# Kernel optimization log

Measured on AMD Instinct MI355X. Metric: run time of the kernel, lower is better.

Reference implementation:

```python
import jax, jax.numpy as jnp
import numpy as np

EPS = 1e-5

def conv2d(x, w, stride=1, padding=0, bias=None):
    out = jax.lax.conv_general_dilated(
        x, w, (stride, stride), [(padding, padding), (padding, padding)],
        dimension_numbers=('NCHW', 'OIHW', 'NCHW'))
    if bias is not None:
        out = out + bias[None, :, None, None]
    return out

def bn_relu(x, gamma, beta, mean, var):
    scale = gamma / jnp.sqrt(var + EPS)
    return jax.nn.relu(x * scale[None, :, None, None]
                       + (beta - mean * scale)[None, :, None, None])

def deform_conv(x, wp, bp, wc, ks, pad, stride):
    # Canonical DeformConv2d (v1, modulation=False) from pytorch-deform-conv-v2.
    b, c, H, W = x.shape
    N = ks * ks
    offset = conv2d(x, wp, stride=stride, padding=1, bias=bp)        # (b,2N,h,w)
    h, w = offset.shape[2], offset.shape[3]
    xp = jnp.pad(x, ((0, 0), (0, 0), (pad, pad), (pad, pad)))        # zero_padding
    Hp, Wp = H + 2 * pad, W + 2 * pad
    off = offset.transpose(0, 2, 3, 1)                               # (b,h,w,2N)
    rng = jnp.arange(-(ks - 1) // 2, (ks - 1) // 2 + 1, dtype=x.dtype)
    pnx, pny = jnp.meshgrid(rng, rng, indexing='ij')
    pnx, pny = pnx.reshape(-1), pny.reshape(-1)                      # (N,)
    p0x = jnp.arange(1, h * stride + 1, stride, dtype=x.dtype)       # torch starts at 1
    p0y = jnp.arange(1, w * stride + 1, stride, dtype=x.dtype)
    px = p0x[None, :, None, None] + pnx[None, None, None, :] + off[..., :N]  # (b,h,w,N)
    py = p0y[None, None, :, None] + pny[None, None, None, :] + off[..., N:]
    qx0 = jnp.floor(jax.lax.stop_gradient(px))
    qy0 = jnp.floor(jax.lax.stop_gradient(py))
    qx0c = jnp.clip(qx0, 0, Hp - 1).astype(jnp.int32)
    qx1c = jnp.clip(qx0 + 1, 0, Hp - 1).astype(jnp.int32)
    qy0c = jnp.clip(qy0, 0, Wp - 1).astype(jnp.int32)
    qy1c = jnp.clip(qy0 + 1, 0, Wp - 1).astype(jnp.int32)
    pxc = jnp.clip(px, 0, Hp - 1)
    pyc = jnp.clip(py, 0, Wp - 1)
    fx0 = qx0c.astype(x.dtype); fx1 = qx1c.astype(x.dtype)
    fy0 = qy0c.astype(x.dtype); fy1 = qy1c.astype(x.dtype)
    g_lt = (1 + (fx0 - pxc)) * (1 + (fy0 - pyc))
    g_rb = (1 - (fx1 - pxc)) * (1 - (fy1 - pyc))
    g_lb = (1 + (fx0 - pxc)) * (1 - (fy1 - pyc))
    g_rt = (1 - (fx1 - pxc)) * (1 + (fy0 - pyc))
    xf = xp.reshape(b, c, Hp * Wp)
    def gather(qx, qy):
        idx = (qx * Wp + qy).reshape(b, 1, h * w * N)
        return jnp.take_along_axis(xf, idx, axis=2).reshape(b, c, h, w, N)
    x_off = (g_lt[:, None] * gather(qx0c, qy0c)
             + g_rb[:, None] * gather(qx1c, qy1c)
             + g_lb[:, None] * gather(qx0c, qy1c)
             + g_rt[:, None] * gather(qx1c, qy0c))                   # (b,c,h,w,N)
    # stride=ks conv over the reshaped (h*ks, w*ks) map == einsum over sample slot n
    return jnp.einsum('bchwn,ocn->bohw', x_off, wc.reshape(wc.shape[0], c, N))

def setup_inputs() -> dict:
    key = jax.random.key(0)
    ks = iter(jax.random.split(key, 40))
    def nrm(shape, scale):
        return jax.random.normal(next(ks), shape, dtype=jnp.float32) * scale
    def he(shape):  # fan_in = prod of all but first dim
        return nrm(shape, float(np.sqrt(2.0 / np.prod(shape[1:]))))
    def bn(c):
        return (jnp.ones((c,), jnp.float32) + nrm((c,), 0.05),  # gamma
                nrm((c,), 0.05),                                 # beta
                nrm((c,), 0.1),                                  # running mean
                jax.random.uniform(next(ks), (c,), jnp.float32, 0.5, 1.5))  # var
    inp = {'x': jax.random.normal(next(ks), (256, 3, 32, 32), dtype=jnp.float32)}
    inp['w1'] = he((32, 3, 3, 3)); inp['b1'] = nrm((32,), 0.01)
    inp['g1'], inp['be1'], inp['m1'], inp['v1'] = bn(32)
    inp['wp2'] = nrm((18, 32, 3, 3), 0.01); inp['bp2'] = nrm((18,), 0.001)
    inp['wc2'] = he((64, 32, 3, 3))
    inp['g2'], inp['be2'], inp['m2'], inp['v2'] = bn(64)
    inp['wp3'] = nrm((18, 64, 3, 3), 0.01); inp['bp3'] = nrm((18,), 0.001)
    inp['wc3'] = he((128, 64, 3, 3))
    inp['g3'], inp['be3'], inp['m3'], inp['v3'] = bn(128)
    inp['wp4'] = nrm((18, 128, 3, 3), 0.01); inp['bp4'] = nrm((18,), 0.001)
    inp['wc4'] = he((128, 128, 3, 3))
    inp['g4'], inp['be4'], inp['m4'], inp['v4'] = bn(128)
    inp['wcls'] = nrm((100, 128), float(1.0 / np.sqrt(128)))
    inp['bcls'] = nrm((100,), 0.01)
    return inp

def reference(x, w1, b1, g1, be1, m1, v1,
              wp2, bp2, wc2, g2, be2, m2, v2,
              wp3, bp3, wc3, g3, be3, m3, v3,
              wp4, bp4, wc4, g4, be4, m4, v4,
              wcls, bcls):
    h = bn_relu(conv2d(x, w1, stride=1, padding=1, bias=b1), g1, be1, m1, v1)   # (b,32,32,32)
    h = bn_relu(deform_conv(h, wp2, bp2, wc2, 3, 1, 2), g2, be2, m2, v2)        # (b,64,16,16)
    h = bn_relu(deform_conv(h, wp3, bp3, wc3, 3, 1, 1), g3, be3, m3, v3)        # (b,128,16,16)
    h = bn_relu(deform_conv(h, wp4, bp4, wc4, 3, 1, 2), g4, be4, m4, v4)        # (b,128,8,8)
    h = jnp.mean(h, axis=(2, 3))                                                # avg_pool2d(8) -> (b,128)
    return h @ wcls.T + bcls[None, :]
```

## Files before the change

### kernel.cpp

```cpp
#include <hip/hip_runtime.h>
#include <math.h>

#define BN_EPS 1e-5f

typedef __attribute__((ext_vector_type(4))) float f4;
typedef __attribute__((ext_vector_type(4))) int i4v;
typedef __attribute__((ext_vector_type(8))) short short8;
typedef __attribute__((ext_vector_type(4))) float f32x4;

__device__ inline unsigned short f2bf(float f) {
    unsigned int u = __builtin_bit_cast(unsigned int, f);
    return (unsigned short)((u + 0x7FFFu + ((u >> 16) & 1u)) >> 16);
}
__device__ inline float blo(int u) { return __builtin_bit_cast(float, (int)(u << 16)); }
__device__ inline float bhi(int u) { return __builtin_bit_cast(float, (int)(u & 0xffff0000)); }
__device__ inline int pkbf_fast(float hi, float lo) {
    unsigned uh = __builtin_bit_cast(unsigned, hi) + 0x8000u;
    unsigned ul = __builtin_bit_cast(unsigned, lo) + 0x8000u;
    return (int)__builtin_amdgcn_perm(uh, ul, 0x07060302u);
}

struct CvtSeg { const float* src; unsigned short* dst; int oreal, c, kpad, end; };
struct CvtArgs { CvtSeg s[7]; };

__global__ __launch_bounds__(256)
void cvt_all(CvtArgs a)
{
    int idx = blockIdx.x * 256 + threadIdx.x;
    int base = 0;
    #pragma unroll
    for (int i = 0; i < 7; ++i) {
        if (idx < a.s[i].end) {
            int local = idx - base;
            int kpad = a.s[i].kpad, c = a.s[i].c;
            int o = local / kpad, k = local - o * kpad;
            unsigned short val = 0;
            if (o < a.s[i].oreal && k < 9 * c) {
                int n = k / c, cc = k - n * c;
                val = f2bf(a.s[i].src[(o * c + cc) * 9 + n]);
            }
            a.s[i].dst[local] = val;
            return;
        }
        base = a.s[i].end;
    }
}

__global__ __launch_bounds__(256)
void conv1_tile(const float* __restrict__ x, const unsigned short* __restrict__ wq,
                const float* __restrict__ bias, const float* __restrict__ g,
                const float* __restrict__ be, const float* __restrict__ m,
                const float* __restrict__ v, unsigned short* __restrict__ out)
{
    __shared__ __align__(16) float img[3072];
    __shared__ __align__(16) unsigned short wt[32 * 40];
    __shared__ float scb[32], shb[32];
    const int tid = threadIdx.x;
    const int b = blockIdx.x >> 2;
    const int qtr = blockIdx.x & 3;
    if (tid < 32) {
        float sc = g[tid] * rsqrtf(v[tid] + BN_EPS);
        scb[tid] = sc;
        shb[tid] = be[tid] - m[tid] * sc + bias[tid] * sc;
    }
    *(ushort4*)&wt[(tid >> 3) * 40 + (tid & 7) * 4] =
        *(const ushort4*)(wq + (tid >> 3) * 32 + (tid & 7) * 4);
    const float* xb = x + (size_t)b * 3072;
    #pragma unroll
    for (int r = 0; r < 3; ++r) {
        int idx = r * 256 + tid;
        *(f4*)&img[idx * 4] = *(const f4*)(xb + idx * 4);
    }
    __syncthreads();
    const int wid = tid >> 6, lane = tid & 63, quad = lane >> 4, m16 = lane & 15;
    short8 af0 = *(const short8*)&wt[m16 * 40 + quad * 8];
    short8 af1 = *(const short8*)&wt[(16 + m16) * 40 + quad * 8];
    #pragma unroll
    for (int it = 0; it < 4; ++it) {
        int pix = qtr * 256 + it * 64 + wid * 16 + m16;
        int i = pix >> 5, j = pix & 31;
        short8 bfrag;
        #pragma unroll
        for (int jj = 0; jj < 8; ++jj) {
            int k = quad * 8 + jj;
            float val = 0.f;
            if (k < 27) {
                int n = k / 3, c = k - n * 3;
                int u = i - 1 + n / 3, vv = j - 1 + n % 3;
                if (u >= 0 && u < 32 && vv >= 0 && vv < 32)
                    val = img[c * 1024 + u * 32 + vv];
            }
            bfrag[jj] = (short)f2bf(val);
        }
        f32x4 a0 = {0.f,0.f,0.f,0.f}, a1 = {0.f,0.f,0.f,0.f};
        a0 = __builtin_amdgcn_mfma_f32_16x16x32_bf16(af0, bfrag, a0, 0, 0, 0);
        a1 = __builtin_amdgcn_mfma_f32_16x16x32_bf16(af1, bfrag, a1, 0, 0, 0);
        unsigned short* op = out + ((size_t)b * 1024 + pix) * 32;
        ushort4 s0, s1;
        #pragma unroll
        for (int rr = 0; rr < 4; ++rr) {
            int o0 = quad * 4 + rr, o1 = 16 + quad * 4 + rr;
            ((unsigned short*)&s0)[rr] = f2bf(fmaxf(fmaf(a0[rr], scb[o0], shb[o0]), 0.f));
            ((unsigned short*)&s1)[rr] = f2bf(fmaxf(fmaf(a1[rr], scb[o1], shb[o1]), 0.f));
        }
        *(ushort4*)(op + quad * 4) = s0;
        *(ushort4*)(op + 16 + quad * 4) = s1;
    }
}

template<int C, int OREAL, int OPAD, int H, int W, int OH, int OW, int S,
         int MTILE, bool DEF, bool BN>
__global__ __launch_bounds__(256, 4)
void dconv(const unsigned short* __restrict__ xact, const float* __restrict__ offp,
           const unsigned short* __restrict__ wq,
           const float* __restrict__ q0, const float* __restrict__ q1,
           const float* __restrict__ q2, const float* __restrict__ q3,
           void* __restrict__ outv)
{
    constexpr int K = C * 9;
    constexpr int KCH = C / 32;
    constexpr int OSPLIT = (OPAD >= 64) ? 4 : 2;
    constexpr int G = 4 / OSPLIT;
    constexpr int OT = OPAD / (16 * OSPLIT);
    constexpr int PW = MTILE / G;
    constexpr int ST = PW / 16;
    constexpr int CP = C + 8;
    constexpr int GL = C / 8;
    constexpr int NGRP = 256 / GL;
    constexpr int OHW = OH * OW;
    constexpr int HWC = H * W * C;
    constexpr int Hp = H + 2, Wp = W + 2;
    static_assert(PW % 16 == 0 && OT >= 1, "tiling");

    __shared__ __align__(16) unsigned short xo[2][MTILE * CP];
    __shared__ __align__(16) i4v tab_i[DEF ? MTILE : 1][9];
    __shared__ __align__(16) f4  tab_w[DEF ? MTILE : 1][9];
    __shared__ int tab_o[DEF ? 1 : MTILE][9];
    __shared__ int tab_m[DEF ? 1 : MTILE][9];
    __shared__ int imgb[MTILE];
    __shared__ float scb[OPAD], shb[OPAD];

    const int tid = threadIdx.x;
    const int p0 = blockIdx.x * MTILE;

    if (tid < MTILE) imgb[tid] = ((p0 + tid) / OHW) * HWC;
    if (BN) {
        for (int o = tid; o < OREAL; o += 256) {
            float sc = q0[o] * rsqrtf(q3[o] + BN_EPS);
            scb[o] = sc;
            shb[o] = q1[o] - q2[o] * sc;
        }
    } else {
        for (int o = tid; o < OREAL; o += 256) scb[o] = q0[o];
    }

    for (int e = tid; e < MTILE * 9; e += 256) {
        int lp = e / 9, n = e % 9;
        int p = p0 + lp;
        int rem = p % OHW;
        int i = rem / OW, j = rem % OW;
        if constexpr (DEF) {
            float ox = offp[(size_t)p * 18 + n];
            float oy = offp[(size_t)p * 18 + 9 + n];
            float px = (float)(i * S + n / 3) + ox;
            float py = (float)(j * S + n % 3) + oy;
            int qx0 = (int)floorf(px), qy0 = (int)floorf(py);
            int x0 = min(max(qx0, 0), Hp - 1), x1 = min(max(qx0 + 1, 0), Hp - 1);
            int y0 = min(max(qy0, 0), Wp - 1), y1 = min(max(qy0 + 1, 0), Wp - 1);
            float pxc = fminf(fmaxf(px, 0.f), (float)(Hp - 1));
            float pyc = fminf(fmaxf(py, 0.f), (float)(Wp - 1));
            float gx0 = 1.f + ((float)x0 - pxc), gx1 = 1.f - ((float)x1 - pxc);
            float gy0 = 1.f + ((float)y0 - pyc), gy1 = 1.f - ((float)y1 - pyc);
            int u0 = x0 - 1, u1 = x1 - 1, v0 = y0 - 1, v1 = y1 - 1;
            bool k0 = (u0 >= 0 && u0 < H && v0 >= 0 && v0 < W);
            bool k1 = (u1 >= 0 && u1 < H && v1 >= 0 && v1 < W);
            bool k2 = (u0 >= 0 && u0 < H && v1 >= 0 && v1 < W);
            bool k3 = (u1 >= 0 && u1 < H && v0 >= 0 && v0 < W);
            i4v ti; f4 tw;
            ti[0] = k0 ? (u0 * W + v0) * C : 0;  tw[0] = k0 ? gx0 * gy0 : 0.f;
            ti[1] = k1 ? (u1 * W + v1) * C : 0;  tw[1] = k1 ? gx1 * gy1 : 0.f;
            ti[2] = k2 ? (u0 * W + v1) * C : 0;  tw[2] = k2 ? gx0 * gy1 : 0.f;
            ti[3] = k3 ? (u1 * W + v0) * C : 0;  tw[3] = k3 ? gx1 * gy0 : 0.f;
            tab_i[lp][n] = ti;
            tab_w[lp][n] = tw;
        } else {
            int u = i * S - 1 + n / 3, vv = j * S - 1 + n % 3;
            bool ok = (u >= 0 && u < H && vv >= 0 && vv < W);
            tab_o[lp][n] = ok ? (u * W + vv) * C : 0;
            tab_m[lp][n] = ok ? -1 : 0;
        }
    }

    const int gl = tid % GL;
    const int grp = tid / GL;
    const int wid = tid >> 6, lane = tid & 63, quad = lane >> 4, m16 = lane & 15;
    const int og = wid % OSPLIT, pg = wid / OSPLIT;
    const int obase = og * OT * 16;
    const int pixbase = pg * PW;

    auto do_gather = [&](int n, int buf) {
        for (int pix = grp; pix < MTILE; pix += NGRP) {
            const unsigned short* xb = xact + imgb[pix] + gl * 8;
            i4v R;
            if constexpr (DEF) {
                i4v ti = tab_i[pix][n];
                f4  tw = tab_w[pix][n];
                i4v A  = *(const i4v*)(xb + ti[0]);
                i4v Bv = *(const i4v*)(xb + ti[1]);
                i4v Cv = *(const i4v*)(xb + ti[2]);
                i4v Dv = *(const i4v*)(xb + ti[3]);
                #pragma unroll
                for (int e2 = 0; e2 < 4; ++e2) {
                    float lo = tw[0] * blo(A[e2]);
                    lo = fmaf(tw[1], blo(Bv[e2]), lo);
                    lo = fmaf(tw[2], blo(Cv[e2]), lo);
                    lo = fmaf(tw[3], blo(Dv[e2]), lo);
                    float hi = tw[0] * bhi(A[e2]);
                    hi = fmaf(tw[1], bhi(Bv[e2]), hi);
                    hi = fmaf(tw[2], bhi(Cv[e2]), hi);
                    hi = fmaf(tw[3], bhi(Dv[e2]), hi);
                    R[e2] = pkbf_fast(hi, lo);
                }
            } else {
                int mask = tab_m[pix][n];
                i4v A = *(const i4v*)(xb + tab_o[pix][n]);
                #pragma unroll
                for (int e2 = 0; e2 < 4; ++e2) R[e2] = A[e2] & mask;
            }
            *(i4v*)&xo[buf][pix * CP + gl * 8] = R;
        }
    };

    auto load_wf = [&](int n, short8 (*wf)[OT]) {
        #pragma unroll
        for (int ch = 0; ch < KCH; ++ch)
            #pragma unroll
            for (int t = 0; t < OT; ++t)
                wf[ch][t] = *(const short8*)(wq + (size_t)(obase + t * 16 + m16) * K
                                             + n * C + ch * 32 + quad * 8);
    };

    f32x4 acc[ST][OT];
    #pragma unroll
    for (int st = 0; st < ST; ++st)
        #pragma unroll
        for (int t = 0; t < OT; ++t) acc[st][t] = (f32x4){0.f, 0.f, 0.f, 0.f};

    short8 wfA[KCH][OT], wfB[KCH][OT];
    __syncthreads();
    do_gather(0, 0);
    load_wf(0, wfA);
    __syncthreads();

    for (int n = 0; n < 9; ++n) {
        const int cur = n & 1;
        if (n < 8) {
            do_gather(n + 1, cur ^ 1);
            load_wf(n + 1, wfB);
        }
        #pragma unroll
        for (int ch = 0; ch < KCH; ++ch)
            #pragma unroll
            for (int st = 0; st < ST; ++st) {
                short8 bf = *(const short8*)&xo[cur][(pixbase + st * 16 + m16) * CP
                                                    + ch * 32 + quad * 8];
                #pragma unroll
                for (int t = 0; t < OT; ++t)
                    acc[st][t] = __builtin_amdgcn_mfma_f32_16x16x32_bf16(
                        wfA[ch][t], bf, acc[st][t], 0, 0, 0);
            }
        if (n < 8) {
            #pragma unroll
            for (int ch = 0; ch < KCH; ++ch)
                #pragma unroll
                for (int t = 0; t < OT; ++t) wfA[ch][t] = wfB[ch][t];
        }
        __syncthreads();
    }

    if constexpr (BN) {
        unsigned short* outw = (unsigned short*)outv;
        #pragma unroll
        for (int st = 0; st < ST; ++st) {
            const int p = p0 + pixbase + st * 16 + m16;
            #pragma unroll
            for (int t = 0; t < OT; ++t) {
                int o = obase + t * 16 + quad * 4;
                ushort4 s;
                #pragma unroll
                for (int rr = 0; rr < 4; ++rr)
                    ((unsigned short*)&s)[rr] =
                        f2bf(fmaxf(fmaf(acc[st][t][rr], scb[o + rr], shb[o + rr]), 0.f));
                *(ushort4*)(outw + (size_t)p * OPAD + o) = s;
            }
        }
    } else {
        float* outf = (float*)outv;
        #pragma unroll
        for (int st = 0; st < ST; ++st) {
            const int p = p0 + pixbase + st * 16 + m16;
            #pragma unroll
            for (int t = 0; t < OT; ++t)
                #pragma unroll
                for (int rr = 0; rr < 4; ++rr) {
                    int o = obase + t * 16 + quad * 4 + rr;
                    if (o < OREAL)
                        outf[(size_t)p * 18 + o] = acc[st][t][rr] + scb[o];
                }
        }
    }
}

__global__ __launch_bounds__(128)
void pool_fc(const unsigned short* __restrict__ h4, const float* __restrict__ wcls,
             const float* __restrict__ bcls, float* __restrict__ out)
{
    __shared__ float pool[128];
    int b = blockIdx.x;
    int tid = threadIdx.x;
    const unsigned short* src = h4 + (size_t)b * 8192;
    float s = 0.f;
    #pragma unroll
    for (int t = 0; t < 64; ++t)
        s += __builtin_bit_cast(float, (unsigned)src[t * 128 + tid] << 16);
    pool[tid] = s * (1.f / 64.f);
    __syncthreads();
    if (tid < 100) {
        float acc = bcls[tid];
        const float* wr = wcls + tid * 128;
        #pragma unroll
        for (int c = 0; c < 128; ++c) acc = fmaf(pool[c], wr[c], acc);
        out[(size_t)b * 100 + tid] = acc;
    }
}

extern "C" void kernel_launch(void* const* d_in, const int* in_sizes, int n_in,
                              void* d_out, int out_size, void* d_ws, size_t ws_size,
                              hipStream_t stream)
{
    const float* x    = (const float*)d_in[0];
    const float* w1   = (const float*)d_in[1];
    const float* b1   = (const float*)d_in[2];
    const float* g1   = (const float*)d_in[3];
    const float* be1  = (const float*)d_in[4];
    const float* m1   = (const float*)d_in[5];
    const float* v1   = (const float*)d_in[6];
    const float* wp2  = (const float*)d_in[7];
    const float* bp2  = (const float*)d_in[8];
    const float* wc2  = (const float*)d_in[9];
    const float* g2   = (const float*)d_in[10];
    const float* be2  = (const float*)d_in[11];
    const float* m2   = (const float*)d_in[12];
    const float* v2   = (const float*)d_in[13];
    const float* wp3  = (const float*)d_in[14];
    const float* bp3  = (const float*)d_in[15];
    const float* wc3  = (const float*)d_in[16];
    const float* g3   = (const float*)d_in[17];
    const float* be3  = (const float*)d_in[18];
    const float* m3   = (const float*)d_in[19];
    const float* v3   = (const float*)d_in[20];
    const float* wp4  = (const float*)d_in[21];
    const float* bp4  = (const float*)d_in[22];
    const float* wc4  = (const float*)d_in[23];
    const float* g4   = (const float*)d_in[24];
    const float* be4  = (const float*)d_in[25];
    const float* m4   = (const float*)d_in[26];
    const float* v4   = (const float*)d_in[27];
    const float* wcls = (const float*)d_in[28];
    const float* bcls = (const float*)d_in[29];
    float* out = (float*)d_out;

    float* ws  = (float*)d_ws;
    float* off = ws;
    unsigned short* h1 = (unsigned short*)(off + 1179648);
    unsigned short* h2 = h1 + 8388608;
    unsigned short* h3 = h2 + 4194304;
    unsigned short* h4 = h3 + 8388608;
    unsigned short* wc2b = h4 + 2097152;
    unsigned short* wc3b = wc2b + 18432;
    unsigned short* wc4b = wc3b + 73728;
    unsigned short* wp2b = wc4b + 147456;
    unsigned short* wp3b = wp2b + 9216;
    unsigned short* wp4b = wp3b + 18432;
    unsigned short* wq1  = wp4b + 36864;
    (void)ws_size; (void)in_sizes; (void)n_in; (void)out_size;

    CvtArgs ca;
    ca.s[0] = { wc2, wc2b, 64, 32, 288, 18432 };
    ca.s[1] = { wc3, wc3b, 128, 64, 576, 92160 };
    ca.s[2] = { wc4, wc4b, 128, 128, 1152, 239616 };
    ca.s[3] = { wp2, wp2b, 18, 32, 288, 248832 };
    ca.s[4] = { wp3, wp3b, 18, 64, 576, 267264 };
    ca.s[5] = { wp4, wp4b, 18, 128, 1152, 304128 };
    ca.s[6] = { w1, wq1, 32, 3, 32, 305152 };
    cvt_all<<<1192, 256, 0, stream>>>(ca);

    conv1_tile<<<1024, 256, 0, stream>>>(x, wq1, b1, g1, be1, m1, v1, h1);

    dconv<32, 18, 32, 32, 32, 16, 16, 2, 32, false, false><<<2048, 256, 0, stream>>>(
        h1, nullptr, wp2b, bp2, nullptr, nullptr, nullptr, off);
    dconv<32, 64, 64, 32, 32, 16, 16, 2, 32, true, true><<<2048, 256, 0, stream>>>(
        h1, off, wc2b, g2, be2, m2, v2, h2);

    dconv<64, 18, 32, 16, 16, 16, 16, 1, 32, false, false><<<2048, 256, 0, stream>>>(
        h2, nullptr, wp3b, bp3, nullptr, nullptr, nullptr, off);
    dconv<64, 128, 128, 16, 16, 16, 16, 1, 32, true, true><<<2048, 256, 0, stream>>>(
        h2, off, wc3b, g3, be3, m3, v3, h3);

    dconv<128, 18, 32, 16, 16, 8, 8, 2, 32, false, false><<<512, 256, 0, stream>>>(
        h3, nullptr, wp4b, bp4, nullptr, nullptr, nullptr, off);
    dconv<128, 128, 128, 16, 16, 8, 8, 2, 16, true, true><<<1024, 256, 0, stream>>>(
        h3, off, wc4b, g4, be4, m4, v4, h4);

    pool_fc<<<256, 128, 0, stream>>>(h4, wcls, bcls, out);
}
```

Measured before the change: 281.1 us.

## Restructure dconv so each wave gathers its own 16-pixel tile without block syncs

Rewrites the deformable-conv kernel so each wave owns a 16-pixel slice: it gathers and bilinearly interpolates its own pixels into a private LDS buffer, which removes the block-wide barriers inside the tap loop. Weight fragments are now read straight from global memory inside the MFMA loop and are no longer prefetched into registers. Non-deformable offset convs skip LDS entirely and feed masked global loads directly into MFMA. Tile sizes and OSPLIT become template parameters, and grids shrink to 64 pixels per block. The trade-off is more repeated weight loads and less weight reuse per wave, in exchange for fewer syncs and a shorter path from gather to MFMA.

```diff
diff --git a/kernel.cpp b/kernel.cpp
--- a/kernel.cpp
+++ b/kernel.cpp
@@ -109,7 +109,7 @@
 }
 
 template<int C, int OREAL, int OPAD, int H, int W, int OH, int OW, int S,
-         int MTILE, bool DEF, bool BN>
+         int OSPLIT, bool DEF, bool BN>
 __global__ __launch_bounds__(256, 4)
 void dconv(const unsigned short* __restrict__ xact, const float* __restrict__ offp,
            const unsigned short* __restrict__ wq,
@@ -119,20 +119,17 @@
 {
     constexpr int K = C * 9;
     constexpr int KCH = C / 32;
-    constexpr int OSPLIT = (OPAD >= 64) ? 4 : 2;
-    constexpr int G = 4 / OSPLIT;
     constexpr int OT = OPAD / (16 * OSPLIT);
-    constexpr int PW = MTILE / G;
-    constexpr int ST = PW / 16;
+    constexpr int NPG = 4 / OSPLIT;
+    constexpr int MTILE = NPG * 16;
     constexpr int CP = C + 8;
-    constexpr int GL = C / 8;
-    constexpr int NGRP = 256 / GL;
+    constexpr bool PIPE = (C <= 64);
+    constexpr int DBUF = (DEF && PIPE) ? 2 : 1;
     constexpr int OHW = OH * OW;
     constexpr int HWC = H * W * C;
     constexpr int Hp = H + 2, Wp = W + 2;
-    static_assert(PW % 16 == 0 && OT >= 1, "tiling");
-
-    __shared__ __align__(16) unsigned short xo[2][MTILE * CP];
+
+    __shared__ __align__(16) unsigned short xo[DEF ? 4 : 1][DBUF][DEF ? 16 * CP : 1];
     __shared__ __align__(16) i4v tab_i[DEF ? MTILE : 1][9];
     __shared__ __align__(16) f4  tab_w[DEF ? MTILE : 1][9];
     __shared__ int tab_o[DEF ? 1 : MTILE][9];
@@ -190,124 +187,123 @@
             tab_m[lp][n] = ok ? -1 : 0;
         }
     }
-
-    const int gl = tid % GL;
-    const int grp = tid / GL;
+    __syncthreads();
+
     const int wid = tid >> 6, lane = tid & 63, quad = lane >> 4, m16 = lane & 15;
     const int og = wid % OSPLIT, pg = wid / OSPLIT;
     const int obase = og * OT * 16;
-    const int pixbase = pg * PW;
-
-    auto do_gather = [&](int n, int buf) {
-        for (int pix = grp; pix < MTILE; pix += NGRP) {
-            const unsigned short* xb = xact + imgb[pix] + gl * 8;
-            i4v R;
-            if constexpr (DEF) {
-                i4v ti = tab_i[pix][n];
-                f4  tw = tab_w[pix][n];
-                i4v A  = *(const i4v*)(xb + ti[0]);
-                i4v Bv = *(const i4v*)(xb + ti[1]);
-                i4v Cv = *(const i4v*)(xb + ti[2]);
-                i4v Dv = *(const i4v*)(xb + ti[3]);
+    const int pl = pg * 16 + m16;
+    const unsigned short* xb0 = xact + imgb[pl];
+
+    f32x4 acc[OT];
+    #pragma unroll
+    for (int t = 0; t < OT; ++t) acc[t] = (f32x4){0.f, 0.f, 0.f, 0.f};
+
+    auto do_mfma = [&](int n, int buf) {
+        #pragma unroll
+        for (int ch = 0; ch < KCH; ++ch) {
+            short8 bf = *(const short8*)&xo[wid][buf][m16 * CP + ch * 32 + quad * 8];
+            #pragma unroll
+            for (int t = 0; t < OT; ++t) {
+                short8 af = *(const short8*)(wq + (size_t)(obase + t * 16 + m16) * K
+                                             + n * C + ch * 32 + quad * 8);
+                acc[t] = __builtin_amdgcn_mfma_f32_16x16x32_bf16(af, bf, acc[t], 0, 0, 0);
+            }
+        }
+    };
+
+    if constexpr (DEF) {
+        i4v T[KCH][4];
+        i4v ti; f4 tw;
+        auto issue = [&](int n) {
+            ti = tab_i[pl][n];
+            tw = tab_w[pl][n];
+            #pragma unroll
+            for (int t = 0; t < KCH; ++t) {
+                const unsigned short* xb = xb0 + (quad + 4 * t) * 8;
+                T[t][0] = *(const i4v*)(xb + ti[0]);
+                T[t][1] = *(const i4v*)(xb + ti[1]);
+                T[t][2] = *(const i4v*)(xb + ti[2]);
+                T[t][3] = *(const i4v*)(xb + ti[3]);
+            }
+        };
+        auto cwrite = [&](int buf) {
+            #pragma unroll
+            for (int t = 0; t < KCH; ++t) {
+                i4v R;
                 #pragma unroll
                 for (int e2 = 0; e2 < 4; ++e2) {
-                    float lo = tw[0] * blo(A[e2]);
-                    lo = fmaf(tw[1], blo(Bv[e2]), lo);
-                    lo = fmaf(tw[2], blo(Cv[e2]), lo);
-                    lo = fmaf(tw[3], blo(Dv[e2]), lo);
-                    float hi = tw[0] * bhi(A[e2]);
-                    hi = fmaf(tw[1], bhi(Bv[e2]), hi);
-                    hi = fmaf(tw[2], bhi(Cv[e2]), hi);
-                    hi = fmaf(tw[3], bhi(Dv[e2]), hi);
+                    float lo = tw[0] * blo(T[t][0][e2]);
+                    lo = fmaf(tw[1], blo(T[t][1][e2]), lo);
+                    lo = fmaf(tw[2], blo(T[t][2][e2]), lo);
+                    lo = fmaf(tw[3], blo(T[t][3][e2]), lo);
+                    float hi = tw[0] * bhi(T[t][0][e2]);
+                    hi = fmaf(tw[1], bhi(T[t][1][e2]), hi);
+                    hi = fmaf(tw[2], bhi(T[t][2][e2]), hi);
+                    hi = fmaf(tw[3], bhi(T[t][3][e2]), hi);
                     R[e2] = pkbf_fast(hi, lo);
                 }
-            } else {
-                int mask = tab_m[pix][n];
-                i4v A = *(const i4v*)(xb + tab_o[pix][n]);
+                *(i4v*)&xo[wid][buf][m16 * CP + (quad + 4 * t) * 8] = R;
+            }
+        };
+        if constexpr (PIPE) {
+            issue(0);
+            cwrite(0);
+            for (int n = 0; n < 9; ++n) {
+                if (n < 8) issue(n + 1);
+                do_mfma(n, n & 1);
+                if (n < 8) cwrite((n + 1) & 1);
+            }
+        } else {
+            for (int n = 0; n < 9; ++n) {
+                issue(n);
+                cwrite(0);
+                do_mfma(n, 0);
+            }
+        }
+    } else {
+        for (int n = 0; n < 9; ++n) {
+            int to = tab_o[pl][n];
+            int mk = tab_m[pl][n];
+            #pragma unroll
+            for (int ch = 0; ch < KCH; ++ch) {
+                i4v B4 = *(const i4v*)(xb0 + to + ch * 32 + quad * 8);
                 #pragma unroll
-                for (int e2 = 0; e2 < 4; ++e2) R[e2] = A[e2] & mask;
-            }
-            *(i4v*)&xo[buf][pix * CP + gl * 8] = R;
-        }
-    };
-
-    auto load_wf = [&](int n, short8 (*wf)[OT]) {
-        #pragma unroll
-        for (int ch = 0; ch < KCH; ++ch)
-            #pragma unroll
-            for (int t = 0; t < OT; ++t)
-                wf[ch][t] = *(const short8*)(wq + (size_t)(obase + t * 16 + m16) * K
-                                             + n * C + ch * 32 + quad * 8);
-    };
-
-    f32x4 acc[ST][OT];
-    #pragma unroll
-    for (int st = 0; st < ST; ++st)
-        #pragma unroll
-        for (int t = 0; t < OT; ++t) acc[st][t] = (f32x4){0.f, 0.f, 0.f, 0.f};
-
-    short8 wfA[KCH][OT], wfB[KCH][OT];
-    __syncthreads();
-    do_gather(0, 0);
-    load_wf(0, wfA);
-    __syncthreads();
-
-    for (int n = 0; n < 9; ++n) {
-        const int cur = n & 1;
-        if (n < 8) {
-            do_gather(n + 1, cur ^ 1);
-            load_wf(n + 1, wfB);
-        }
-        #pragma unroll
-        for (int ch = 0; ch < KCH; ++ch)
-            #pragma unroll
-            for (int st = 0; st < ST; ++st) {
-                short8 bf = *(const short8*)&xo[cur][(pixbase + st * 16 + m16) * CP
-                                                    + ch * 32 + quad * 8];
+                for (int e2 = 0; e2 < 4; ++e2) B4[e2] &= mk;
+                short8 bf = __builtin_bit_cast(short8, B4);
                 #pragma unroll
-                for (int t = 0; t < OT; ++t)
-                    acc[st][t] = __builtin_amdgcn_mfma_f32_16x16x32_bf16(
-                        wfA[ch][t], bf, acc[st][t], 0, 0, 0);
-            }
-        if (n < 8) {
-            #pragma unroll
-            for (int ch = 0; ch < KCH; ++ch)
-                #pragma unroll
-                for (int t = 0; t < OT; ++t) wfA[ch][t] = wfB[ch][t];
-        }
-        __syncthreads();
-    }
-
+                for (int t = 0; t < OT; ++t) {
+                    short8 af = *(const short8*)(wq + (size_t)(obase + t * 16 + m16) * K
+                                                 + n * C + ch * 32 + quad * 8);
+                    acc[t] = __builtin_amdgcn_mfma_f32_16x16x32_bf16(af, bf, acc[t], 0, 0, 0);
+                }
+            }
+        }
+    }
+
+    const int p = p0 + pl;
     if constexpr (BN) {
         unsigned short* outw = (unsigned short*)outv;
         #pragma unroll
-        for (int st = 0; st < ST; ++st) {
-            const int p = p0 + pixbase + st * 16 + m16;
-            #pragma unroll
-            for (int t = 0; t < OT; ++t) {
-                int o = obase + t * 16 + quad * 4;
-                ushort4 s;
-                #pragma unroll
-                for (int rr = 0; rr < 4; ++rr)
-                    ((unsigned short*)&s)[rr] =
-                        f2bf(fmaxf(fmaf(acc[st][t][rr], scb[o + rr], shb[o + rr]), 0.f));
-                *(ushort4*)(outw + (size_t)p * OPAD + o) = s;
-            }
+        for (int t = 0; t < OT; ++t) {
+            int o = obase + t * 16 + quad * 4;
+            ushort4 s;
+            #pragma unroll
+            for (int rr = 0; rr < 4; ++rr)
+                ((unsigned short*)&s)[rr] =
+                    f2bf(fmaxf(fmaf(acc[t][rr], scb[o + rr], shb[o + rr]), 0.f));
+            *(ushort4*)(outw + (size_t)p * OPAD + o) = s;
         }
     } else {
         float* outf = (float*)outv;
         #pragma unroll
-        for (int st = 0; st < ST; ++st) {
-            const int p = p0 + pixbase + st * 16 + m16;
-            #pragma unroll
-            for (int t = 0; t < OT; ++t)
-                #pragma unroll
-                for (int rr = 0; rr < 4; ++rr) {
-                    int o = obase + t * 16 + quad * 4 + rr;
-                    if (o < OREAL)
-                        outf[(size_t)p * 18 + o] = acc[st][t][rr] + scb[o];
-                }
-        }
+        for (int t = 0; t < OT; ++t)
+            #pragma unroll
+            for (int rr = 0; rr < 4; ++rr) {
+                int o = obase + t * 16 + quad * 4 + rr;
+                if (o < OREAL)
+                    outf[(size_t)p * 18 + o] = acc[t][rr] + scb[o];
+            }
     }
 }
 
@@ -397,19 +393,19 @@
 
     conv1_tile<<<1024, 256, 0, stream>>>(x, wq1, b1, g1, be1, m1, v1, h1);
 
-    dconv<32, 18, 32, 32, 32, 16, 16, 2, 32, false, false><<<2048, 256, 0, stream>>>(
+    dconv<32, 18, 32, 32, 32, 16, 16, 2, 1, false, false><<<1024, 256, 0, stream>>>(
         h1, nullptr, wp2b, bp2, nullptr, nullptr, nullptr, off);
-    dconv<32, 64, 64, 32, 32, 16, 16, 2, 32, true, true><<<2048, 256, 0, stream>>>(
+    dconv<32, 64, 64, 32, 32, 16, 16, 2, 1, true, true><<<1024, 256, 0, stream>>>(
         h1, off, wc2b, g2, be2, m2, v2, h2);
 
-    dconv<64, 18, 32, 16, 16, 16, 16, 1, 32, false, false><<<2048, 256, 0, stream>>>(
+    dconv<64, 18, 32, 16, 16, 16, 16, 1, 1, false, false><<<1024, 256, 0, stream>>>(
         h2, nullptr, wp3b, bp3, nullptr, nullptr, nullptr, off);
-    dconv<64, 128, 128, 16, 16, 16, 16, 1, 32, true, true><<<2048, 256, 0, stream>>>(
+    dconv<64, 128, 128, 16, 16, 16, 16, 1, 1, true, true><<<1024, 256, 0, stream>>>(
         h2, off, wc3b, g3, be3, m3, v3, h3);
 
-    dconv<128, 18, 32, 16, 16, 8, 8, 2, 32, false, false><<<512, 256, 0, stream>>>(
+    dconv<128, 18, 32, 16, 16, 8, 8, 2, 1, false, false><<<256, 256, 0, stream>>>(
         h3, nullptr, wp4b, bp4, nullptr, nullptr, nullptr, off);
-    dconv<128, 128, 128, 16, 16, 8, 8, 2, 16, true, true><<<1024, 256, 0, stream>>>(
+    dconv<128, 128, 128, 16, 16, 8, 8, 2, 2, true, true><<<512, 256, 0, stream>>>(
         h3, off, wc4b, g4, be4, m4, v4, h4);
 
     pool_fc<<<256, 128, 0, stream>>>(h4, wcls, bcls, out);
```

New measurement: 375.8 us. 1.34x slower.
